# Optimization experiments

Measured on AMD Instinct MI355X. Metric: run time of the kernel, lower is better.

Reference implementation:

```python
import jax, jax.numpy as jnp
import numpy as np
import math

N_FFT = 1024
HOP = 256
N_FRAMES = 16384
SR = 24000
FFT_BIN = N_FFT // 2 + 1
EPS = 1e-11


def hann(n):
    # torch.hann_window default (periodic=True)
    return 0.5 * (1.0 - jnp.cos(2.0 * jnp.pi * jnp.arange(n, dtype=jnp.float32) / n))


def linear_interp(x, scale):
    # x: [B, T] -> [B, T*scale]; matches F.interpolate(mode='linear', align_corners=False)
    T = x.shape[-1]
    pos = (jnp.arange(T * scale, dtype=jnp.float32) + 0.5) / scale - 0.5
    pos = jnp.clip(pos, 0.0, T - 1.0)
    lo = jnp.floor(pos).astype(jnp.int32)
    hi = jnp.minimum(lo + 1, T - 1)
    frac = pos - lo.astype(jnp.float32)
    return x[:, lo] * (1.0 - frac) + x[:, hi] * frac


def impulse_train(f0, hop_length, sample_rate):
    # f0: [B, n_frames] -> impulse train [B, n_frames*hop]
    f0_up = linear_interp(f0, hop_length)
    phase = jnp.cumsum(f0_up, axis=-1) / sample_rate
    saw = jnp.mod(phase, 1.0)
    imp = saw - jnp.roll(saw, -1, axis=-1) + f0_up / sample_rate
    # original runs under torch.no_grad()
    return jax.lax.stop_gradient(imp)


def stft(x, n_fft, hop, window):
    # torch.stft(center=True, pad_mode='reflect', onesided, normalized=False)
    pad = n_fft // 2
    xp = jnp.pad(x, ((0, 0), (pad, pad)), mode="reflect")
    nf = (xp.shape[-1] - n_fft) // hop + 1
    idx = jnp.arange(nf)[:, None] * hop + jnp.arange(n_fft)[None, :]
    frames = xp[:, idx] * window  # [B, nf, n_fft]
    return jnp.fft.rfft(frames, axis=-1).transpose(0, 2, 1)  # [B, bins, nf]


def istft(S, n_fft, hop, window):
    # torch.istft(center=True): windowed overlap-add, divide by sum of squared windows
    B = S.shape[0]
    frames = jnp.fft.irfft(S.transpose(0, 2, 1), n=n_fft, axis=-1) * window  # [B, nf, n_fft]
    nf = frames.shape[1]
    out_len = n_fft + (nf - 1) * hop
    idx = jnp.arange(nf)[:, None] * hop + jnp.arange(n_fft)[None, :]
    sig = jnp.zeros((B, out_len), frames.dtype).at[:, idx].add(frames)
    wsq = jnp.zeros((out_len,), frames.dtype).at[idx].add(
        jnp.broadcast_to(window * window, (nf, n_fft))
    )
    pad = n_fft // 2
    return sig[:, pad:-pad] / jnp.maximum(wsq[pad:-pad], EPS)


def spectral_envelope_filter(signal, envelope, n_fft, hop):
    w = hann(n_fft)
    S = stft(signal, n_fft, hop, w)[:, :, 1:]  # drop first frame -> [B, bins, n_frames]
    return istft(S * envelope, n_fft, hop, w)


def estimate_minimum_phase(amp):
    # amp: [B, bins, T] real positive envelope; cepstral min-phase along dim 1
    n = (amp.shape[1] - 1) * 2
    cep = jnp.fft.irfft(jnp.log(amp), n=n, axis=1)
    fold = jnp.concatenate(
        [jnp.ones((1,), jnp.float32),
         2.0 * jnp.ones((n // 2 - 1,), jnp.float32),
         jnp.ones((1,), jnp.float32),
         jnp.zeros((n // 2 - 1,), jnp.float32)]
    )
    cep = cep * fold[None, :, None]
    return jnp.exp(jnp.fft.rfft(cep, axis=1))  # complex min-phase spectrum [B, bins, T]


def setup_inputs() -> dict:
    key = jax.random.key(0)
    k1, k2, k3 = jax.random.split(key, 3)
    log_f0 = jnp.full((1, N_FRAMES), math.log(100.0), dtype=jnp.float32)
    spec_env_noi = jax.random.normal(k1, (1, FFT_BIN, N_FRAMES), jnp.float32) - 6.0
    spec_env_per = jax.random.normal(k2, (1, FFT_BIN, N_FRAMES), jnp.float32) - 6.0
    noise = jax.random.normal(k3, (1, HOP * N_FRAMES), jnp.float32)
    return {"log_f0": log_f0, "spec_env_noi": spec_env_noi,
            "spec_env_per": spec_env_per, "noise": noise}


def reference(log_f0, spec_env_noi, spec_env_per, noise):
    pulse = impulse_train(jnp.exp(log_f0), HOP, SR)
    noi = spectral_envelope_filter(noise, jnp.exp(spec_env_noi), N_FFT, HOP)
    per = spectral_envelope_filter(
        pulse, estimate_minimum_phase(jnp.exp(spec_env_per)), N_FFT, HOP
    )
    return noi + per  # [1, (N_FRAMES-1)*HOP]
```

## Files before the change

kernel.cpp:

```cpp
#include <hip/hip_runtime.h>
#include <math.h>

#define L_TOT 4194304
#define NFR   16384
#define OUTN  4194048


__device__ __forceinline__ int lvl_off(int a) {
  return L_TOT - (L_TOT >> (a - 1));
}

__device__ __forceinline__ int swz(int e) {
  int h = (e >> 4) & 3, g = (e >> 6) & 3, f = (e >> 8) & 3;
  return e ^ (h * 5) ^ (g * 3) ^ ((f * 12) & 15);
}

__device__ __forceinline__ int dr4(int p) {
  return ((p & 3) << 8) | (((p >> 2) & 3) << 6) | (((p >> 4) & 3) << 4) |
         (((p >> 6) & 3) << 2) | ((p >> 8) & 3);
}

__device__ __forceinline__ float f0_up_val(const float* f0arr, int j) {
  float pos = __fadd_rn(__fmul_rn(__fadd_rn((float)j, 0.5f), 1.0f / 256.0f), -0.5f);
  pos = fminf(fmaxf(pos, 0.0f), 16383.0f);
  int lo = (int)pos;
  int hi = min(lo + 1, NFR - 1);
  float frac = __fadd_rn(pos, -(float)lo);
  float a = __fmul_rn(f0arr[lo], __fadd_rn(1.0f, -frac));
  float b = __fmul_rn(f0arr[hi], frac);
  return __fadd_rn(a, b);
}

__device__ __forceinline__ float f0_up_local(const float* Fl, int w0, int j) {
  float pos = __fadd_rn(__fmul_rn(__fadd_rn((float)j, 0.5f), 1.0f / 256.0f), -0.5f);
  pos = fminf(fmaxf(pos, 0.0f), 16383.0f);
  int lo = (int)pos;
  int hi = min(lo + 1, NFR - 1);
  float frac = __fadd_rn(pos, -(float)lo);
  float a = __fmul_rn(Fl[lo - w0], __fadd_rn(1.0f, -frac));
  float b = __fmul_rn(Fl[hi - w0], frac);
  return __fadd_rn(a, b);
}

__device__ float prefix_sum(const float* W, const float* f0arr, int m) {
  float acc = 0.0f;
  bool first = true;
  int pos = 0;
  for (int a = 22; a >= 1; --a) {
    if (m & (1 << a)) {
      float node = W[lvl_off(a) + (pos >> a)];
      acc = first ? node : __fadd_rn(acc, node);
      first = false;
      pos += (1 << a);
    }
  }
  if (m & 1) {
    float node = f0_up_val(f0arr, pos);
    acc = first ? node : __fadd_rn(acc, node);
  }
  return acc;
}

__global__ __launch_bounds__(256) void tree_kernel(const float* __restrict__ logf0,
                                                   float* __restrict__ W) {
  int tid = threadIdx.x;
  if (blockIdx.x < 72) {
    int g = blockIdx.x * 256 + tid;
    float* twc = W + 2 * L_TOT;
    float* tws = twc + 512;
    float* f0arr = twc + 2048;
    if (g < 512) {
      double a = (double)g * 3.14159265358979323846 / 512.0;
      twc[g] = (float)cos(a);
      tws[g] = (float)sin(a);
    }
    if (g >= 2048 && g < 2048 + NFR) {
      f0arr[g - 2048] = (float)exp((double)logf0[g - 2048]);
    }
  }
  __shared__ float Fl[10];
  __shared__ float A[2048];
  __shared__ float B[1024];
  int base = blockIdx.x * 2048;
  int w0 = (base >> 8) - 1;
  if (tid < 10) {
    int f = min(max(w0 + tid, 0), NFR - 1);
    Fl[tid] = (float)exp((double)logf0[f]);
  }
  __syncthreads();
  for (int i = tid; i < 2048; i += 256) A[i] = f0_up_local(Fl, w0, base + i);
  __syncthreads();
  float* src = A;
  float* dst = B;
  int cnt = 1024;
  for (int a = 1; a <= 11; ++a) {
    int gbase = base >> a;
    for (int i = tid; i < cnt; i += 256) {
      float v = __fadd_rn(src[2 * i], src[2 * i + 1]);
      dst[i] = v;
      if (a == 11) W[lvl_off(11) + gbase + i] = v;
    }
    __syncthreads();
    float* tmp = src; src = dst; dst = tmp;
    cnt >>= 1;
  }
}

__global__ __launch_bounds__(256) void tree_top_kernel(float* W) {
  __shared__ float A[2048];
  __shared__ float B[1024];
  int tid = threadIdx.x;
  for (int i = tid; i < 2048; i += 256) A[i] = W[lvl_off(11) + i];
  __syncthreads();
  float* src = A;
  float* dst = B;
  int cnt = 1024;
  for (int a = 12; a <= 22; ++a) {
    for (int i = tid; i < cnt; i += 256) {
      float v = __fadd_rn(src[2 * i], src[2 * i + 1]);
      dst[i] = v;
      W[lvl_off(a) + i] = v;
    }
    __syncthreads();
    float* tmp = src; src = dst; dst = tmp;
    cnt >>= 1;
  }
  const float* f0arr = W + 2 * L_TOT + 2048;
  for (int b = tid; b < 1024; b += 256) {
    W[2 * b] = prefix_sum(W, f0arr, 4096 * (b + 1));
    int m2 = 4096 * b + 4097;
    W[2 * b + 1] = (m2 <= L_TOT) ? prefix_sum(W, f0arr, m2) : 0.0f;
  }
}

__global__ __launch_bounds__(256) void pulse_kernel(float* W) {
  const float* f0arr = W + 2 * L_TOT + 2048;
  __shared__ float Tl[510];
  __shared__ float P[4100];
  int tid = threadIdx.x;
  int base = blockIdx.x * 4096;

  float v[16];
#pragma unroll
  for (int c = 0; c < 16; ++c) v[c] = f0_up_val(f0arr, base + 16 * tid + c);
  float s2[8], s4[4], s8[2];
#pragma unroll
  for (int j = 0; j < 8; ++j) s2[j] = __fadd_rn(v[2 * j], v[2 * j + 1]);
#pragma unroll
  for (int j = 0; j < 4; ++j) s4[j] = __fadd_rn(s2[2 * j], s2[2 * j + 1]);
  s8[0] = __fadd_rn(s4[0], s4[1]);
  s8[1] = __fadd_rn(s4[2], s4[3]);
  Tl[tid] = __fadd_rn(s8[0], s8[1]);
  __syncthreads();
  if (tid < 128) Tl[256 + tid] = __fadd_rn(Tl[2 * tid], Tl[2 * tid + 1]);
  __syncthreads();
  if (tid < 64)  Tl[384 + tid] = __fadd_rn(Tl[256 + 2 * tid], Tl[256 + 2 * tid + 1]);
  __syncthreads();
  if (tid < 32)  Tl[448 + tid] = __fadd_rn(Tl[384 + 2 * tid], Tl[384 + 2 * tid + 1]);
  __syncthreads();
  if (tid < 16)  Tl[480 + tid] = __fadd_rn(Tl[448 + 2 * tid], Tl[448 + 2 * tid + 1]);
  __syncthreads();
  if (tid < 8)   Tl[496 + tid] = __fadd_rn(Tl[480 + 2 * tid], Tl[480 + 2 * tid + 1]);
  __syncthreads();
  if (tid < 4)   Tl[504 + tid] = __fadd_rn(Tl[496 + 2 * tid], Tl[496 + 2 * tid + 1]);
  __syncthreads();
  if (tid < 2)   Tl[508 + tid] = __fadd_rn(Tl[504 + 2 * tid], Tl[504 + 2 * tid + 1]);
  __syncthreads();

  float accT = 0.0f;
  bool firstT = true;
  {
    int pos = 0;
    for (int a = 22; a >= 12; --a) {
      if (base & (1 << a)) {
        float node = W[lvl_off(a) + (pos >> a)];
        accT = firstT ? node : __fadd_rn(accT, node);
        firstT = false;
        pos += (1 << a);
      }
    }
  }
  float accM = accT;
  bool firstM = firstT;
  {
    int rh = 16 * tid;
    int lpos = 0;
    for (int a = 11; a >= 4; --a) {
      if (rh & (1 << a)) {
        float node = Tl[512 - (512 >> (a - 4)) + (lpos >> a)];
        accM = firstM ? node : __fadd_rn(accM, node);
        firstM = false;
        lpos += (1 << a);
      }
    }
  }
  if (tid >= 1) P[16 * tid] = accM;
#pragma unroll
  for (int c = 1; c <= 15; ++c) {
    float acc = accM;
    bool first = firstM;
    int lp = 0;
    if (c & 8) { float n = s8[lp >> 3]; acc = first ? n : __fadd_rn(acc, n); first = false; lp += 8; }
    if (c & 4) { float n = s4[lp >> 2]; acc = first ? n : __fadd_rn(acc, n); first = false; lp += 4; }
    if (c & 2) { float n = s2[lp >> 1]; acc = first ? n : __fadd_rn(acc, n); first = false; lp += 2; }
    if (c & 1) { float n = v[lp];       acc = first ? n : __fadd_rn(acc, n); }
    P[16 * tid + c] = acc;
  }
  if (tid == 0) P[4096] = W[2 * blockIdx.x];
  if (tid == 1) P[4097] = W[2 * blockIdx.x + 1];
  __syncthreads();

  float o[16];
#pragma unroll
  for (int c = 0; c < 16; ++c) {
    int i = base + 16 * tid + c;
    float P1 = P[16 * tid + c + 1];
    float P2 = (i == L_TOT - 1) ? prefix_sum(W, f0arr, 1)
                                : P[16 * tid + c + 2];
    float t1 = __fdiv_rn(P1, 24000.0f);
    float saw1 = __fadd_rn(t1, -floorf(t1));
    float t2 = __fdiv_rn(P2, 24000.0f);
    float saw2 = __fadd_rn(t2, -floorf(t2));
    float cc = __fdiv_rn(v[c], 24000.0f);
    o[c] = __fadd_rn(__fadd_rn(saw1, -saw2), cc);
  }
#pragma unroll
  for (int k = 0; k < 4; ++k)
    *(float4*)&W[L_TOT + base + 16 * tid + 4 * k] =
        make_float4(o[4 * k], o[4 * k + 1], o[4 * k + 2], o[4 * k + 3]);
}

template <int DIR>
__device__ __forceinline__ void bfly_dif(float2* F, int e0, int e1, int e2, int e3,
                                         float ur, float ui) {
  if (DIR < 0) ui = -ui;
  float2 x0 = F[e0], x1 = F[e1], x2 = F[e2], x3 = F[e3];
  float s0r = x0.x + x2.x, s0i = x0.y + x2.y;
  float s1r = x1.x + x3.x, s1i = x1.y + x3.y;
  float d0r = x0.x - x2.x, d0i = x0.y - x2.y;
  float ddr = x1.x - x3.x, ddi = x1.y - x3.y;
  float t3r = (DIR > 0) ? -ddi : ddi;
  float t3i = (DIR > 0) ? ddr : -ddr;
  float vr = ur * ur - ui * ui, vi = 2.0f * ur * ui;
  float w3r = ur * vr - ui * vi, w3i = ur * vi + ui * vr;
  F[e0] = make_float2(s0r + s1r, s0i + s1i);
  float a1r = d0r + t3r, a1i = d0i + t3i;
  F[e1] = make_float2(a1r * ur - a1i * ui, a1r * ui + a1i * ur);
  float a2r = s0r - s1r, a2i = s0i - s1i;
  F[e2] = make_float2(a2r * vr - a2i * vi, a2r * vi + a2i * vr);
  float a3r = d0r - t3r, a3i = d0i - t3i;
  F[e3] = make_float2(a3r * w3r - a3i * w3i, a3r * w3i + a3i * w3r);
  __syncthreads();
}

template <int DIR>
__device__ __forceinline__ void bfly_dit(float2* F, int e0, int e1, int e2, int e3,
                                         float ur, float ui) {
  if (DIR < 0) ui = -ui;
  float2 x0 = F[e0], x1 = F[e1], x2 = F[e2], x3 = F[e3];
  float vr = ur * ur - ui * ui, vi = 2.0f * ur * ui;
  float w3r = ur * vr - ui * vi, w3i = ur * vi + ui * vr;
  float b1r = x1.x * ur - x1.y * ui, b1i = x1.x * ui + x1.y * ur;
  float b2r = x2.x * vr - x2.y * vi, b2i = x2.x * vi + x2.y * vr;
  float b3r = x3.x * w3r - x3.y * w3i, b3i = x3.x * w3i + x3.y * w3r;
  float s0r = x0.x + b2r, s0i = x0.y + b2i;
  float d0r = x0.x - b2r, d0i = x0.y - b2i;
  float s1r = b1r + b3r, s1i = b1i + b3i;
  float ddr = b1r - b3r, ddi = b1i - b3i;
  float d1r = (DIR > 0) ? -ddi : ddi;
  float d1i = (DIR > 0) ? ddr : -ddr;
  F[e0] = make_float2(s0r + s1r, s0i + s1i);
  F[e1] = make_float2(d0r + d1r, d0i + d1i);
  F[e2] = make_float2(s0r - s1r, s0i - s1i);
  F[e3] = make_float2(d0r - d1r, d0i - d1i);
  __syncthreads();
}

__device__ __forceinline__ float hann_w(int i, const float2* T0) {
  int j = (i > 512) ? (1024 - i) : i;
  float c = (j <= 256) ? T0[j].x : -T0[512 - j].x;
  return 0.5f - 0.5f * c;
}

__device__ __forceinline__ float edge_scale(int t, const float2* T0) {
  int p = t + 512;
  int jmin = max(0, (p - 768) >> 8);
  int jmax = min(NFR - 1, p >> 8);
  float wsq = 0.0f;
  for (int j = jmin; j <= jmax; ++j) {
    float w = hann_w(p - 256 * j, T0);
    wsq += w * w;
  }
  return 1.5f / fmaxf(wsq, 1e-11f);
}

__device__ __forceinline__ void combine_one(int k, float An, const float2* F, float2* H) {
  int k2 = (1024 - k) & 1023;
  float2 z = F[swz(dr4(k))], mm = F[swz(dr4(k2))];
  float Ar = 0.5f * (z.x + mm.x), Ai = 0.5f * (z.y - mm.y);
  float Br = 0.5f * (z.y + mm.y), Bi = 0.5f * (mm.x - z.x);
  float2 h = H[k];
  H[k] = make_float2(Br * h.x - Bi * h.y + Ar * An,
                     Br * h.y + Bi * h.x + Ai * An);
}

__global__ __launch_bounds__(256) void column_kernel(
    const float* __restrict__ noise,
    const float* __restrict__ envn,
    const float* __restrict__ envp,
    const float* __restrict__ W,
    float* __restrict__ out) {
  __shared__ float2 F[1024];
  __shared__ float2 hA[513], hB[513];
  __shared__ float2 TW[341];
  int tid = threadIdx.x;
  int bid = blockIdx.x;
  int g = (bid & 7) * 1024 + (bid >> 3);
  int fA = 2 * g;
  const float* pulse = W + L_TOT;
  const float* gtab = W + 2 * L_TOT;
  const float2* T0 = TW;
  const float2* T1 = TW + 257;
  const float2* T2 = TW + 321;
  const float2* T3 = TW + 337;

  for (int i = tid; i < 341; i += 256) {
    int e;
    if (i < 257) e = i;
    else if (i < 321) e = (i - 257) << 2;
    else if (i < 337) e = (i - 321) << 4;
    else e = (i - 337) << 6;
    TW[i] = make_float2(gtab[e], gtab[512 + e]);
  }
  for (int k = tid; k < 513; k += 256) {
    float2 e = *(const float2*)&envp[k * NFR + fA];
    hA[k] = e;
  }

  int a00 = swz(tid), a01 = swz(tid + 256), a02 = swz(tid + 512), a03 = swz(tid + 768);
  int b1_ = ((tid >> 6) << 8) | (tid & 63);
  int a10 = swz(b1_), a11 = swz(b1_ + 64), a12 = swz(b1_ + 128), a13 = swz(b1_ + 192);
  int b2_ = ((tid >> 4) << 6) | (tid & 15);
  int a20 = swz(b2_), a21 = swz(b2_ + 16), a22 = swz(b2_ + 32), a23 = swz(b2_ + 48);
  int b3_ = ((tid >> 2) << 4) | (tid & 3);
  int a30 = swz(b3_), a31 = swz(b3_ + 4), a32 = swz(b3_ + 8), a33 = swz(b3_ + 12);
  int q_ = tid << 2;
  int a40 = swz(q_), a41 = swz(q_ + 1), a42 = swz(q_ + 2), a43 = swz(q_ + 3);
  __syncthreads();

  F[a00] = hA[tid];
  F[a01] = hA[tid + 256];
  F[a02] = (tid == 0) ? hA[512] : hA[512 - tid];
  F[a03] = hA[256 - tid];
  __syncthreads();
  { float2 t_ = T0[tid];      bfly_dif<+1>(F, a00, a01, a02, a03, t_.x, t_.y); }
  { float2 t_ = T1[tid & 63]; bfly_dif<+1>(F, a10, a11, a12, a13, t_.x, t_.y); }
  { float2 t_ = T2[tid & 15]; bfly_dif<+1>(F, a20, a21, a22, a23, t_.x, t_.y); }
  { float2 t_ = T3[tid & 3];  bfly_dif<+1>(F, a30, a31, a32, a33, t_.x, t_.y); }
  {
    int drt = ((tid & 3) << 6) | (((tid >> 2) & 3) << 4) |
              (((tid >> 4) & 3) << 2) | ((tid >> 6) & 3);
    float2 x0 = F[a40], x1 = F[a41], x2 = F[a42], x3 = F[a43];
    float s0r = x0.x + x2.x, s0i = x0.y + x2.y;
    float s1r = x1.x + x3.x, s1i = x1.y + x3.y;
    float d0r = x0.x - x2.x, d0i = x0.y - x2.y;
    float ddr = x1.x - x3.x, ddi = x1.y - x3.y;
    float y0r = s0r + s1r, y0i = s0i + s1i;
    float y1r = d0r - ddi, y1i = d0i + ddr;
    float y2r = s0r - s1r, y2i = s0i - s1i;
    float sc0 = (drt == 0) ? (1.0f / 1024.0f) : (2.0f / 1024.0f);
    float sc2 = (drt == 0) ? (1.0f / 1024.0f) : 0.0f;
    y0r *= sc0; y0i *= sc0;
    y1r *= (2.0f / 1024.0f); y1i *= (2.0f / 1024.0f);
    y2r *= sc2; y2i *= sc2;
    float S0r = y0r + y2r, S0i = y0i + y2i;
    float D0r = y0r - y2r, D0i = y0i - y2i;
    float D1r = y1i, D1i = -y1r;
    F[a40] = make_float2(S0r + y1r, S0i + y1i);
    F[a41] = make_float2(D0r + D1r, D0i + D1i);
    F[a42] = make_float2(S0r - y1r, S0i - y1i);
    F[a43] = make_float2(D0r - D1r, D0i - D1i);
  }
  __syncthreads();
  { float2 t_ = T3[tid & 3];  bfly_dit<-1>(F, a30, a31, a32, a33, t_.x, t_.y); }
  { float2 t_ = T2[tid & 15]; bfly_dit<-1>(F, a20, a21, a22, a23, t_.x, t_.y); }
  { float2 t_ = T1[tid & 63]; bfly_dit<-1>(F, a10, a11, a12, a13, t_.x, t_.y); }
  { float2 t_ = T0[tid];      bfly_dit<-1>(F, a00, a01, a02, a03, t_.x, t_.y); }
  {
    int k2 = (1024 - tid) & 1023;
    float2 z = F[a00], mm = F[swz(k2)];
    float GAr = 0.5f * (z.x + mm.x), GAi = 0.5f * (z.y - mm.y);
    float GBr = 0.5f * (z.y + mm.y), GBi = 0.5f * (mm.x - z.x);
    float er = expf(GAr);
    float si, co;
    sincosf(GAi, &si, &co);
    hA[tid] = make_float2(er * co, er * si);
    er = expf(GBr);
    sincosf(GBi, &si, &co);
    hB[tid] = make_float2(er * co, er * si);

    z = F[a01]; mm = F[swz(768 - tid)];
    GAr = 0.5f * (z.x + mm.x); GAi = 0.5f * (z.y - mm.y);
    GBr = 0.5f * (z.y + mm.y); GBi = 0.5f * (mm.x - z.x);
    er = expf(GAr);
    sincosf(GAi, &si, &co);
    hA[tid + 256] = make_float2(er * co, er * si);
    er = expf(GBr);
    sincosf(GBi, &si, &co);
    hB[tid + 256] = make_float2(er * co, er * si);

    if (tid == 0) {
      z = F[a02];
      GAr = 0.5f * (z.x + z.x); GAi = 0.0f;
      GBr = 0.5f * (z.y + z.y); GBi = 0.0f;
      er = expf(GAr);
      sincosf(GAi, &si, &co);
      hA[512] = make_float2(er * co, er * si);
      er = expf(GBr);
      sincosf(GBi, &si, &co);
      hB[512] = make_float2(er * co, er * si);
    }
  }
  __syncthreads();

#define PACK_FRAME(QOFF, J, ADDR)                                      \
  {                                                                    \
    int i = tid + 256 * (J);                                           \
    int q = (QOFF) + i;                                                \
    if (q < 0) q = -q;                                                 \
    else if (q >= L_TOT) q = 2 * L_TOT - 2 - q;                        \
    float wv = hann_w(i, T0);                                          \
    F[ADDR] = make_float2(noise[q] * wv, pulse[q] * wv);               \
  }
  PACK_FRAME(256 * fA - 256, 0, a00)
  PACK_FRAME(256 * fA - 256, 1, a01)
  PACK_FRAME(256 * fA - 256, 2, a02)
  PACK_FRAME(256 * fA - 256, 3, a03)
  __syncthreads();
  { float2 t_ = T0[tid];      bfly_dif<-1>(F, a00, a01, a02, a03, t_.x, t_.y); }
  { float2 t_ = T1[tid & 63]; bfly_dif<-1>(F, a10, a11, a12, a13, t_.x, t_.y); }
  { float2 t_ = T2[tid & 15]; bfly_dif<-1>(F, a20, a21, a22, a23, t_.x, t_.y); }
  { float2 t_ = T3[tid & 3];  bfly_dif<-1>(F, a30, a31, a32, a33, t_.x, t_.y); }
  bfly_dif<-1>(F, a40, a41, a42, a43, 1.0f, 0.0f);
  float2 eA0 = *(const float2*)&envn[tid * NFR + fA];
  combine_one(tid, expf(eA0.x), F, hA);
  float2 eA1 = *(const float2*)&envn[(tid + 256) * NFR + fA];
  combine_one(tid + 256, expf(eA1.x), F, hA);
  float2 eA2 = make_float2(0.0f, 0.0f);
  if (tid == 0) {
    eA2 = *(const float2*)&envn[512 * NFR + fA];
    combine_one(512, expf(eA2.x), F, hA);
  }
  __syncthreads();

  PACK_FRAME(256 * fA, 0, a00)
  PACK_FRAME(256 * fA, 1, a01)
  PACK_FRAME(256 * fA, 2, a02)
  PACK_FRAME(256 * fA, 3, a03)
  __syncthreads();
  { float2 t_ = T0[tid];      bfly_dif<-1>(F, a00, a01, a02, a03, t_.x, t_.y); }
  { float2 t_ = T1[tid & 63]; bfly_dif<-1>(F, a10, a11, a12, a13, t_.x, t_.y); }
  { float2 t_ = T2[tid & 15]; bfly_dif<-1>(F, a20, a21, a22, a23, t_.x, t_.y); }
  { float2 t_ = T3[tid & 3];  bfly_dif<-1>(F, a30, a31, a32, a33, t_.x, t_.y); }
  bfly_dif<-1>(F, a40, a41, a42, a43, 1.0f, 0.0f);
  combine_one(tid, expf(eA0.y), F, hB);
  combine_one(tid + 256, expf(eA1.y), F, hB);
  if (tid == 0) combine_one(512, expf(eA2.y), F, hB);
  __syncthreads();

#pragma unroll
  for (int j = 0; j < 4; ++j) {
    int i = tid + 256 * j;
    float2 zv;
    if (i <= 512) {
      zv = make_float2(hA[i].x - hB[i].y, hA[i].y + hB[i].x);
    } else {
      int jj = 1024 - i;
      zv = make_float2(hA[jj].x + hB[jj].y, hB[jj].x - hA[jj].y);
    }
    F[swz(dr4(i))] = zv;
  }
  __syncthreads();
  bfly_dit<+1>(F, a40, a41, a42, a43, 1.0f, 0.0f);
  { float2 t_ = T3[tid & 3];  bfly_dit<+1>(F, a30, a31, a32, a33, t_.x, t_.y); }
  { float2 t_ = T2[tid & 15]; bfly_dit<+1>(F, a20, a21, a22, a23, t_.x, t_.y); }
  { float2 t_ = T1[tid & 63]; bfly_dit<+1>(F, a10, a11, a12, a13, t_.x, t_.y); }
  { float2 t_ = T0[tid];      bfly_dit<+1>(F, a00, a01, a02, a03, t_.x, t_.y); }
  const float scl = 1.0f / 1536.0f;
  {
    float2 f0v = F[a00], f1v = F[a01], f2v = F[a02], f3v = F[a03];
    float hw0 = hann_w(tid, T0) * scl;
    float hw1 = hann_w(tid + 256, T0) * scl;
    float hw2 = hann_w(tid + 512, T0) * scl;
    float hw3 = hann_w(tid + 768, T0) * scl;
    int tb = 256 * fA - 512 + tid;
    float val;
    int t;
    t = tb;
    val = f0v.x * hw0;
    if (t >= 0) {
      if (t < 256) val *= edge_scale(t, T0);
      atomicAdd(&out[t], val);
    }
    t = tb + 256;
    val = f1v.x * hw1 + f0v.y * hw0;
    if (t >= 0 && t < OUTN) {
      if (t < 256 || t >= OUTN - 256) val *= edge_scale(t, T0);
      atomicAdd(&out[t], val);
    }
    t = tb + 512;
    val = f2v.x * hw2 + f1v.y * hw1;
    if (t < OUTN) {
      if (t < 256 || t >= OUTN - 256) val *= edge_scale(t, T0);
      atomicAdd(&out[t], val);
    }
    t = tb + 768;
    val = f3v.x * hw3 + f2v.y * hw2;
    if (t < OUTN) {
      if (t >= OUTN - 256) val *= edge_scale(t, T0);
      atomicAdd(&out[t], val);
    }
    t = tb + 1024;
    val = f3v.y * hw3;
    if (t < OUTN) {
      if (t >= OUTN - 256) val *= edge_scale(t, T0);
      atomicAdd(&out[t], val);
    }
  }
#undef PACK_FRAME
}

extern "C" void kernel_launch(void* const* d_in, const int* in_sizes, int n_in,
                              void* d_out, int out_size, void* d_ws, size_t ws_size,
                              hipStream_t stream) {
  const float* logf0 = (const float*)d_in[0];
  const float* envn  = (const float*)d_in[1];
  const float* envp  = (const float*)d_in[2];
  const float* noise = (const float*)d_in[3];
  float* out = (float*)d_out;
  float* W = (float*)d_ws;

  tree_kernel<<<dim3(2048), dim3(256), 0, stream>>>(logf0, W);
  tree_top_kernel<<<dim3(1), dim3(256), 0, stream>>>(W);
  pulse_kernel<<<dim3(L_TOT / 4096), dim3(256), 0, stream>>>(W);
  hipMemsetAsync(d_out, 0, (size_t)out_size * sizeof(float), stream);
  column_kernel<<<dim3(NFR / 2), dim3(256), 0, stream>>>(noise, envn, envp, W, out);
}
```

Before: 244.0 us.

## Fuse tree, top, pulse and memset into one cooperative kernel with grid syncs

Merges the three prefix-sum stages (block tree reduction, single-block top reduction, pulse generation) and the output memset into one cooperative kernel of 1024 blocks, using grid-wide syncs in place of kernel boundaries. Each block now handles two 2048-sample tree chunks, and the per-block boundary prefix sums move from the single top block into the pulse phase. This removes several launch gaps and the separate memset. In exchange it adds grid-sync overhead, and the single-block top phase now idles the whole grid; 1024 co-resident blocks must also fit on the device.

```diff
diff --git a/kernel.cpp b/kernel.cpp
--- a/kernel.cpp
+++ b/kernel.cpp
@@ -1,5 +1,8 @@
 #include <hip/hip_runtime.h>
+#include <hip/hip_cooperative_groups.h>
 #include <math.h>
+
+namespace cg = cooperative_groups;
 
 #define L_TOT 4194304
 #define NFR   16384
@@ -61,173 +64,185 @@
   return acc;
 }
 
-__global__ __launch_bounds__(256) void tree_kernel(const float* __restrict__ logf0,
-                                                   float* __restrict__ W) {
+__global__ __launch_bounds__(256) void prep_kernel(const float* __restrict__ logf0,
+                                                   float* __restrict__ W,
+                                                   float* __restrict__ out) {
   int tid = threadIdx.x;
-  if (blockIdx.x < 72) {
-    int g = blockIdx.x * 256 + tid;
-    float* twc = W + 2 * L_TOT;
-    float* tws = twc + 512;
-    float* f0arr = twc + 2048;
-    if (g < 512) {
-      double a = (double)g * 3.14159265358979323846 / 512.0;
-      twc[g] = (float)cos(a);
-      tws[g] = (float)sin(a);
-    }
-    if (g >= 2048 && g < 2048 + NFR) {
-      f0arr[g - 2048] = (float)exp((double)logf0[g - 2048]);
-    }
-  }
-  __shared__ float Fl[10];
-  __shared__ float A[2048];
-  __shared__ float B[1024];
-  int base = blockIdx.x * 2048;
-  int w0 = (base >> 8) - 1;
-  if (tid < 10) {
-    int f = min(max(w0 + tid, 0), NFR - 1);
-    Fl[tid] = (float)exp((double)logf0[f]);
-  }
-  __syncthreads();
-  for (int i = tid; i < 2048; i += 256) A[i] = f0_up_local(Fl, w0, base + i);
-  __syncthreads();
-  float* src = A;
-  float* dst = B;
-  int cnt = 1024;
-  for (int a = 1; a <= 11; ++a) {
-    int gbase = base >> a;
-    for (int i = tid; i < cnt; i += 256) {
-      float v = __fadd_rn(src[2 * i], src[2 * i + 1]);
-      dst[i] = v;
-      if (a == 11) W[lvl_off(11) + gbase + i] = v;
-    }
-    __syncthreads();
-    float* tmp = src; src = dst; dst = tmp;
-    cnt >>= 1;
-  }
-}
-
-__global__ __launch_bounds__(256) void tree_top_kernel(float* W) {
-  __shared__ float A[2048];
-  __shared__ float B[1024];
-  int tid = threadIdx.x;
-  for (int i = tid; i < 2048; i += 256) A[i] = W[lvl_off(11) + i];
-  __syncthreads();
-  float* src = A;
-  float* dst = B;
-  int cnt = 1024;
-  for (int a = 12; a <= 22; ++a) {
-    for (int i = tid; i < cnt; i += 256) {
-      float v = __fadd_rn(src[2 * i], src[2 * i + 1]);
-      dst[i] = v;
-      W[lvl_off(a) + i] = v;
-    }
-    __syncthreads();
-    float* tmp = src; src = dst; dst = tmp;
-    cnt >>= 1;
-  }
-  const float* f0arr = W + 2 * L_TOT + 2048;
-  for (int b = tid; b < 1024; b += 256) {
-    W[2 * b] = prefix_sum(W, f0arr, 4096 * (b + 1));
-    int m2 = 4096 * b + 4097;
-    W[2 * b + 1] = (m2 <= L_TOT) ? prefix_sum(W, f0arr, m2) : 0.0f;
-  }
-}
-
-__global__ __launch_bounds__(256) void pulse_kernel(float* W) {
-  const float* f0arr = W + 2 * L_TOT + 2048;
-  __shared__ float Tl[510];
-  __shared__ float P[4100];
-  int tid = threadIdx.x;
-  int base = blockIdx.x * 4096;
-
-  float v[16];
-#pragma unroll
-  for (int c = 0; c < 16; ++c) v[c] = f0_up_val(f0arr, base + 16 * tid + c);
-  float s2[8], s4[4], s8[2];
-#pragma unroll
-  for (int j = 0; j < 8; ++j) s2[j] = __fadd_rn(v[2 * j], v[2 * j + 1]);
-#pragma unroll
-  for (int j = 0; j < 4; ++j) s4[j] = __fadd_rn(s2[2 * j], s2[2 * j + 1]);
-  s8[0] = __fadd_rn(s4[0], s4[1]);
-  s8[1] = __fadd_rn(s4[2], s4[3]);
-  Tl[tid] = __fadd_rn(s8[0], s8[1]);
-  __syncthreads();
-  if (tid < 128) Tl[256 + tid] = __fadd_rn(Tl[2 * tid], Tl[2 * tid + 1]);
-  __syncthreads();
-  if (tid < 64)  Tl[384 + tid] = __fadd_rn(Tl[256 + 2 * tid], Tl[256 + 2 * tid + 1]);
-  __syncthreads();
-  if (tid < 32)  Tl[448 + tid] = __fadd_rn(Tl[384 + 2 * tid], Tl[384 + 2 * tid + 1]);
-  __syncthreads();
-  if (tid < 16)  Tl[480 + tid] = __fadd_rn(Tl[448 + 2 * tid], Tl[448 + 2 * tid + 1]);
-  __syncthreads();
-  if (tid < 8)   Tl[496 + tid] = __fadd_rn(Tl[480 + 2 * tid], Tl[480 + 2 * tid + 1]);
-  __syncthreads();
-  if (tid < 4)   Tl[504 + tid] = __fadd_rn(Tl[496 + 2 * tid], Tl[496 + 2 * tid + 1]);
-  __syncthreads();
-  if (tid < 2)   Tl[508 + tid] = __fadd_rn(Tl[504 + 2 * tid], Tl[504 + 2 * tid + 1]);
-  __syncthreads();
-
-  float accT = 0.0f;
-  bool firstT = true;
+  int bid = blockIdx.x;
+  __shared__ union SU {
+    struct { float A[2048]; float B[1024]; float Fl[10]; } t;
+    struct { float Tl[510]; float P[4100]; } p;
+  } U;
+
+  float* twc = W + 2 * L_TOT;
+  float* tws = twc + 512;
+  float* f0arr = twc + 2048;
+
+  if (bid < 2) {
+    int g = bid * 256 + tid;
+    double a = (double)g * 3.14159265358979323846 / 512.0;
+    twc[g] = (float)cos(a);
+    tws[g] = (float)sin(a);
+  }
+  if (bid >= 2 && bid < 66) {
+    int g = (bid - 2) * 256 + tid;
+    f0arr[g] = (float)exp((double)logf0[g]);
+  }
   {
-    int pos = 0;
-    for (int a = 22; a >= 12; --a) {
-      if (base & (1 << a)) {
-        float node = W[lvl_off(a) + (pos >> a)];
-        accT = firstT ? node : __fadd_rn(accT, node);
-        firstT = false;
-        pos += (1 << a);
+    int base_o = bid * 4096;
+#pragma unroll
+    for (int k = 0; k < 4; ++k) {
+      int off = base_o + k * 1024 + tid * 4;
+      if (off < OUTN) *(float4*)&out[off] = make_float4(0.f, 0.f, 0.f, 0.f);
+    }
+  }
+  for (int rep = 0; rep < 2; ++rep) {
+    int base = (2 * bid + rep) * 2048;
+    int w0 = (base >> 8) - 1;
+    __syncthreads();
+    if (tid < 10) {
+      int f = min(max(w0 + tid, 0), NFR - 1);
+      U.t.Fl[tid] = (float)exp((double)logf0[f]);
+    }
+    __syncthreads();
+    for (int i = tid; i < 2048; i += 256) U.t.A[i] = f0_up_local(U.t.Fl, w0, base + i);
+    __syncthreads();
+    float* src = U.t.A;
+    float* dst = U.t.B;
+    int cnt = 1024;
+    for (int a = 1; a <= 11; ++a) {
+      int gbase = base >> a;
+      for (int i = tid; i < cnt; i += 256) {
+        float v = __fadd_rn(src[2 * i], src[2 * i + 1]);
+        dst[i] = v;
+        if (a == 11) W[lvl_off(11) + gbase + i] = v;
       }
-    }
-  }
-  float accM = accT;
-  bool firstM = firstT;
+      __syncthreads();
+      float* tmp = src; src = dst; dst = tmp;
+      cnt >>= 1;
+    }
+  }
+
+  cg::this_grid().sync();
+
+  if (bid == 0) {
+    for (int i = tid; i < 2048; i += 256) U.t.A[i] = W[lvl_off(11) + i];
+    __syncthreads();
+    float* src = U.t.A;
+    float* dst = U.t.B;
+    int cnt = 1024;
+    for (int a = 12; a <= 22; ++a) {
+      for (int i = tid; i < cnt; i += 256) {
+        float v = __fadd_rn(src[2 * i], src[2 * i + 1]);
+        dst[i] = v;
+        W[lvl_off(a) + i] = v;
+      }
+      __syncthreads();
+      float* tmp = src; src = dst; dst = tmp;
+      cnt >>= 1;
+    }
+  }
+
+  cg::this_grid().sync();
+
   {
-    int rh = 16 * tid;
-    int lpos = 0;
-    for (int a = 11; a >= 4; --a) {
-      if (rh & (1 << a)) {
-        float node = Tl[512 - (512 >> (a - 4)) + (lpos >> a)];
-        accM = firstM ? node : __fadd_rn(accM, node);
-        firstM = false;
-        lpos += (1 << a);
+    float* Tl = U.p.Tl;
+    float* P = U.p.P;
+    int base = bid * 4096;
+
+    float v[16];
+#pragma unroll
+    for (int c = 0; c < 16; ++c) v[c] = f0_up_val(f0arr, base + 16 * tid + c);
+    float s2[8], s4[4], s8[2];
+#pragma unroll
+    for (int j = 0; j < 8; ++j) s2[j] = __fadd_rn(v[2 * j], v[2 * j + 1]);
+#pragma unroll
+    for (int j = 0; j < 4; ++j) s4[j] = __fadd_rn(s2[2 * j], s2[2 * j + 1]);
+    s8[0] = __fadd_rn(s4[0], s4[1]);
+    s8[1] = __fadd_rn(s4[2], s4[3]);
+    __syncthreads();
+    Tl[tid] = __fadd_rn(s8[0], s8[1]);
+    __syncthreads();
+    if (tid < 128) Tl[256 + tid] = __fadd_rn(Tl[2 * tid], Tl[2 * tid + 1]);
+    __syncthreads();
+    if (tid < 64)  Tl[384 + tid] = __fadd_rn(Tl[256 + 2 * tid], Tl[256 + 2 * tid + 1]);
+    __syncthreads();
+    if (tid < 32)  Tl[448 + tid] = __fadd_rn(Tl[384 + 2 * tid], Tl[384 + 2 * tid + 1]);
+    __syncthreads();
+    if (tid < 16)  Tl[480 + tid] = __fadd_rn(Tl[448 + 2 * tid], Tl[448 + 2 * tid + 1]);
+    __syncthreads();
+    if (tid < 8)   Tl[496 + tid] = __fadd_rn(Tl[480 + 2 * tid], Tl[480 + 2 * tid + 1]);
+    __syncthreads();
+    if (tid < 4)   Tl[504 + tid] = __fadd_rn(Tl[496 + 2 * tid], Tl[496 + 2 * tid + 1]);
+    __syncthreads();
+    if (tid < 2)   Tl[508 + tid] = __fadd_rn(Tl[504 + 2 * tid], Tl[504 + 2 * tid + 1]);
+    __syncthreads();
+
+    float accT = 0.0f;
+    bool firstT = true;
+    {
+      int pos = 0;
+      for (int a = 22; a >= 12; --a) {
+        if (base & (1 << a)) {
+          float node = W[lvl_off(a) + (pos >> a)];
+          accT = firstT ? node : __fadd_rn(accT, node);
+          firstT = false;
+          pos += (1 << a);
+        }
       }
     }
-  }
-  if (tid >= 1) P[16 * tid] = accM;
-#pragma unroll
-  for (int c = 1; c <= 15; ++c) {
-    float acc = accM;
-    bool first = firstM;
-    int lp = 0;
-    if (c & 8) { float n = s8[lp >> 3]; acc = first ? n : __fadd_rn(acc, n); first = false; lp += 8; }
-    if (c & 4) { float n = s4[lp >> 2]; acc = first ? n : __fadd_rn(acc, n); first = false; lp += 4; }
-    if (c & 2) { float n = s2[lp >> 1]; acc = first ? n : __fadd_rn(acc, n); first = false; lp += 2; }
-    if (c & 1) { float n = v[lp];       acc = first ? n : __fadd_rn(acc, n); }
-    P[16 * tid + c] = acc;
-  }
-  if (tid == 0) P[4096] = W[2 * blockIdx.x];
-  if (tid == 1) P[4097] = W[2 * blockIdx.x + 1];
-  __syncthreads();
-
-  float o[16];
-#pragma unroll
-  for (int c = 0; c < 16; ++c) {
-    int i = base + 16 * tid + c;
-    float P1 = P[16 * tid + c + 1];
-    float P2 = (i == L_TOT - 1) ? prefix_sum(W, f0arr, 1)
-                                : P[16 * tid + c + 2];
-    float t1 = __fdiv_rn(P1, 24000.0f);
-    float saw1 = __fadd_rn(t1, -floorf(t1));
-    float t2 = __fdiv_rn(P2, 24000.0f);
-    float saw2 = __fadd_rn(t2, -floorf(t2));
-    float cc = __fdiv_rn(v[c], 24000.0f);
-    o[c] = __fadd_rn(__fadd_rn(saw1, -saw2), cc);
-  }
-#pragma unroll
-  for (int k = 0; k < 4; ++k)
-    *(float4*)&W[L_TOT + base + 16 * tid + 4 * k] =
-        make_float4(o[4 * k], o[4 * k + 1], o[4 * k + 2], o[4 * k + 3]);
+    float accM = accT;
+    bool firstM = firstT;
+    {
+      int rh = 16 * tid;
+      int lpos = 0;
+      for (int a = 11; a >= 4; --a) {
+        if (rh & (1 << a)) {
+          float node = Tl[512 - (512 >> (a - 4)) + (lpos >> a)];
+          accM = firstM ? node : __fadd_rn(accM, node);
+          firstM = false;
+          lpos += (1 << a);
+        }
+      }
+    }
+    if (tid >= 1) P[16 * tid] = accM;
+#pragma unroll
+    for (int c = 1; c <= 15; ++c) {
+      float acc = accM;
+      bool first = firstM;
+      int lp = 0;
+      if (c & 8) { float n = s8[lp >> 3]; acc = first ? n : __fadd_rn(acc, n); first = false; lp += 8; }
+      if (c & 4) { float n = s4[lp >> 2]; acc = first ? n : __fadd_rn(acc, n); first = false; lp += 4; }
+      if (c & 2) { float n = s2[lp >> 1]; acc = first ? n : __fadd_rn(acc, n); first = false; lp += 2; }
+      if (c & 1) { float n = v[lp];       acc = first ? n : __fadd_rn(acc, n); }
+      P[16 * tid + c] = acc;
+    }
+    if (tid == 0) P[4096] = prefix_sum(W, f0arr, base + 4096);
+    if (tid == 1) {
+      int m2 = base + 4097;
+      P[4097] = (m2 <= L_TOT) ? prefix_sum(W, f0arr, m2) : 0.0f;
+    }
+    __syncthreads();
+
+    float o[16];
+#pragma unroll
+    for (int c = 0; c < 16; ++c) {
+      int i = base + 16 * tid + c;
+      float P1 = P[16 * tid + c + 1];
+      float P2 = (i == L_TOT - 1) ? prefix_sum(W, f0arr, 1)
+                                  : P[16 * tid + c + 2];
+      float t1 = __fdiv_rn(P1, 24000.0f);
+      float saw1 = __fadd_rn(t1, -floorf(t1));
+      float t2 = __fdiv_rn(P2, 24000.0f);
+      float saw2 = __fadd_rn(t2, -floorf(t2));
+      float cc = __fdiv_rn(v[c], 24000.0f);
+      o[c] = __fadd_rn(__fadd_rn(saw1, -saw2), cc);
+    }
+#pragma unroll
+    for (int k = 0; k < 4; ++k)
+      *(float4*)&W[L_TOT + base + 16 * tid + 4 * k] =
+          make_float4(o[4 * k], o[4 * k + 1], o[4 * k + 2], o[4 * k + 3]);
+  }
 }
 
 template <int DIR>
@@ -540,9 +555,8 @@
   float* out = (float*)d_out;
   float* W = (float*)d_ws;
 
-  tree_kernel<<<dim3(2048), dim3(256), 0, stream>>>(logf0, W);
-  tree_top_kernel<<<dim3(1), dim3(256), 0, stream>>>(W);
-  pulse_kernel<<<dim3(L_TOT / 4096), dim3(256), 0, stream>>>(W);
-  hipMemsetAsync(d_out, 0, (size_t)out_size * sizeof(float), stream);
+  void* args[] = {(void*)&logf0, (void*)&W, (void*)&out};
+  hipLaunchCooperativeKernel((const void*)prep_kernel, dim3(1024), dim3(256),
+                             args, 0, stream);
   column_kernel<<<dim3(NFR / 2), dim3(256), 0, stream>>>(noise, envn, envp, W, out);
 }
```

New measurement: 461.5 us. 89.1% more time.
